# Kernel tuning notes

Measured on AMD Instinct MI355X. Metric: run time of the kernel, lower is better.

The kernel has to match this reference:

```python
import jax, jax.numpy as jnp
import numpy as np

B, L, PATCH_IN, D, NPOS = 64, 1024, 768, 1152, 256


def setup_inputs() -> dict:
    key = jax.random.key(0)
    k1, k2, k3, k4 = jax.random.split(key, 4)
    pixel_values = jax.random.normal(k1, (B, L, PATCH_IN), dtype=jnp.float32)
    # per-sample (h, w) with h*w <= L and h, w >= 16 (pure upsampling of 16x16 grid)
    hs = np.array([16 + (i % 17) for i in range(B)], dtype=np.int64)
    ws = (L // hs).astype(np.int64)
    spatial_shapes = jnp.asarray(np.stack([hs, ws], axis=1))
    W = jax.random.normal(k2, (D, PATCH_IN), dtype=jnp.float32) * 0.02
    b = jax.random.normal(k3, (D,), dtype=jnp.float32) * 0.02
    pos_emb = jax.random.normal(k4, (NPOS, D), dtype=jnp.float32) * 0.02
    return {"pixel_values": pixel_values, "spatial_shapes": spatial_shapes,
            "W": W, "b": b, "pos_emb": pos_emb}


def _resized_pos_embeddings(pos_emb, spatial_shapes_np, max_length):
    # pos_emb: [num_patches, D] -> [G, G, D] grid
    g = int(np.sqrt(pos_emb.shape[0]))
    d = pos_emb.shape[1]
    grid = pos_emb.reshape(g, g, d)
    rows = []
    for i in range(spatial_shapes_np.shape[0]):
        h, w = int(spatial_shapes_np[i, 0]), int(spatial_shapes_np[i, 1])
        # half-pixel bilinear == torch F.interpolate(align_corners=False); antialias
        # is a no-op for upsampling (h, w >= g)
        r = jax.image.resize(grid, (h, w, d), method="bilinear").reshape(h * w, d)
        pad = jnp.broadcast_to(r[0], (max_length - h * w, d))  # replicate first patch
        rows.append(jnp.concatenate([r, pad], axis=0))
    return jnp.stack(rows)  # [B, max_length, D]


def reference(pixel_values, spatial_shapes, W, b, pos_emb):
    # patch linear embedding: [B, L, Cpp] x [D, Cpp] -> [B, L, D]
    patch_embeds = jnp.einsum("blk,dk->bld", pixel_values, W) + b
    ss = np.asarray(spatial_shapes)  # static per-sample shapes
    pos = _resized_pos_embeddings(pos_emb, ss, pixel_values.shape[1])
    return patch_embeds + pos
```

## Files before the change

kernel.cpp:

```cpp
#include <hip/hip_runtime.h>

typedef __bf16 bf16x8 __attribute__((ext_vector_type(8)));
typedef float  f32x4  __attribute__((ext_vector_type(4)));

constexpr int BM = 128, BN = 128, BK = 32;
constexpr int MDIM = 65536, NDIM = 1152, KDIM = 768;
constexpr int NBN = NDIM / BN;
constexpr int NKT = KDIM / BK;
constexpr int GRID = (MDIM / BM) * NBN;
constexpr int LDSROWB = BK * 2;

__device__ __forceinline__ void gload16(const void* g, void* l) {
  __builtin_amdgcn_global_load_lds(
      (const __attribute__((address_space(1))) void*)g,
      (__attribute__((address_space(3))) void*)l, 16, 0, 0);
}

__device__ __forceinline__ unsigned pk2(float x, float y) {
  __bf16 a = (__bf16)x, b = (__bf16)y;
  return (unsigned)__builtin_bit_cast(unsigned short, a) |
         ((unsigned)__builtin_bit_cast(unsigned short, b) << 16);
}

__global__ __launch_bounds__(256)
void repack_kernel(const float* __restrict__ in, __bf16* __restrict__ out) {
  const int c    = blockIdx.x * 256 + threadIdx.x;
  const int c_in = c & 511;
  const int img  = c >> 9;
  const int kt   = img % NKT;
  const int pan  = img / NKT;
  const int o = c_in * 16;
  const int u = (o >> 6) & 7;
  const int a = o ^ ((u ^ (u >> 2)) << 4);
  const int r = a >> 6;
  const int p = (a >> 4) & 3;
  const float* src = in + (size_t)(pan * 128 + r) * KDIM + kt * 32 + p * 8;
  const float4 x = *reinterpret_cast<const float4*>(src);
  const float4 y = *reinterpret_cast<const float4*>(src + 4);
  uint4 r4;
  r4.x = pk2(x.x, x.y); r4.y = pk2(x.z, x.w);
  r4.z = pk2(y.x, y.y); r4.w = pk2(y.z, y.w);
  *reinterpret_cast<uint4*>(out + (size_t)c * 8) = r4;
}

__global__ __launch_bounds__(256, 3)
void gemm_swz2_kernel(const __bf16* __restrict__ Aimg,
                      const __bf16* __restrict__ Bimg,
                      const int*   __restrict__ ss,
                      const float* __restrict__ bias,
                      const float* __restrict__ pos,
                      float* __restrict__ out) {
  __shared__ __align__(16) unsigned char SM[32768];
  __bf16* As0 = reinterpret_cast<__bf16*>(SM);
  __bf16* Bs0 = reinterpret_cast<__bf16*>(SM + 16384);
  float*  Cs  = reinterpret_cast<float*>(SM);

  const int tid  = threadIdx.x;
  const int lane = tid & 63;
  const int wid  = tid >> 6;
  const int wr   = wid >> 1;
  const int wc   = wid & 1;

  const int bidh = blockIdx.x;
  const int bid  = (bidh & 7) * (GRID / 8) + (bidh >> 3);
  const int bm   = bid / NBN;
  const int bn   = bid % NBN;

  auto stage = [&](int kt, int buf) {
    const __bf16* wsA = Aimg + ((size_t)(bm * NKT + kt) << 12);
    const __bf16* wsB = Bimg + ((size_t)(bn * NKT + kt) << 12);
    char* la = (char*)As0 + buf * 8192;
    char* lb = (char*)Bs0 + buf * 8192;
    gload16(wsA + tid * 8,         la + tid * 16);
    gload16(wsA + (256 + tid) * 8, la + (256 + tid) * 16);
    gload16(wsB + tid * 8,         lb + tid * 16);
    gload16(wsB + (256 + tid) * 8, lb + (256 + tid) * 16);
  };

  f32x4 acc[4][4];
#pragma unroll
  for (int i = 0; i < 4; ++i)
#pragma unroll
    for (int j = 0; j < 4; ++j) acc[i][j] = (f32x4)0.0f;

  const int fr = lane & 15;
  const int kg = lane >> 4;
  const int abase = (((wr * 64 + fr) * LDSROWB) + kg * 16) ^ ((fr & 7) << 4);
  const int bbase = (((wc * 64 + fr) * LDSROWB) + kg * 16) ^ ((fr & 7) << 4);

  auto compute = [&](int buf) {
    const char* pa = (const char*)As0 + buf * 8192;
    const char* pb = (const char*)Bs0 + buf * 8192;
    bf16x8 af[4], bfv[4];
#pragma unroll
    for (int mf = 0; mf < 4; ++mf)
      af[mf] = *reinterpret_cast<const bf16x8*>(pa + abase + mf * 16 * LDSROWB);
#pragma unroll
    for (int nf = 0; nf < 4; ++nf)
      bfv[nf] = *reinterpret_cast<const bf16x8*>(pb + bbase + nf * 16 * LDSROWB);
#pragma unroll
    for (int mf = 0; mf < 4; ++mf)
#pragma unroll
      for (int nf = 0; nf < 4; ++nf)
        acc[mf][nf] = __builtin_amdgcn_mfma_f32_16x16x32_bf16(af[mf], bfv[nf], acc[mf][nf], 0, 0, 0);
  };

  stage(0, 0);
  for (int kt = 0; kt < NKT; ++kt) {
    const int cur = kt & 1;
    __syncthreads();
    if (kt + 1 < NKT) stage(kt + 1, cur ^ 1);
    compute(cur);
  }

  const int chunk = tid & 15;
  const int gcol  = bn * BN + chunk * 8;
  const f32x4 bias_lo = *reinterpret_cast<const f32x4*>(bias + gcol);
  const f32x4 bias_hi = *reinterpret_cast<const f32x4*>(bias + gcol + 4);

  const int s  = bm >> 3;
  const int h  = ss[2 * s];
  const int w  = ss[2 * s + 1];
  const int hw = h * w;
  const float rh = 16.0f / (float)h;
  const float rw = 16.0f / (float)w;

#pragma unroll
  for (int half = 0; half < 2; ++half) {
    __syncthreads();
#pragma unroll
    for (int mm = 0; mm < 2; ++mm) {
#pragma unroll
      for (int nf = 0; nf < 4; ++nf) {
#pragma unroll
        for (int rg = 0; rg < 4; ++rg) {
          const int rowL = wr * 32 + mm * 16 + kg * 4 + rg;
          const int col  = wc * 64 + nf * 16 + fr;
          const int key  = (rowL & 3) ^ ((rowL >> 2) & 3);
          Cs[(rowL << 7) + (col ^ (key << 3))] = acc[half * 2 + mm][nf][rg];
        }
      }
    }
    __syncthreads();
#pragma unroll
    for (int pass = 0; pass < 4; ++pass) {
      const int rowL = pass * 16 + (tid >> 4);
      const int key  = (rowL & 3) ^ ((rowL >> 2) & 3);
      const float* crow = Cs + (rowL << 7) + ((chunk ^ key) << 3);
      const f32x4 c0 = *reinterpret_cast<const f32x4*>(crow);
      const f32x4 c1 = *reinterpret_cast<const f32x4*>(crow + 4);

      const int grow = bm * BM + (rowL >> 5) * 64 + half * 32 + (rowL & 31);
      int p = grow & 1023;
      if (p >= hw) p = 0;
      const int y = p / w;
      const int x = p - y * w;
      const float fy = ((float)y + 0.5f) * rh - 0.5f;
      const float fx = ((float)x + 0.5f) * rw - 0.5f;
      const float yf = floorf(fy), xf = floorf(fx);
      const float ty = fy - yf,   tx = fx - xf;
      int iy0 = (int)yf, ix0 = (int)xf;
      int iy1 = iy0 + 1 > 15 ? 15 : iy0 + 1;
      int ix1 = ix0 + 1 > 15 ? 15 : ix0 + 1;
      iy0 = iy0 < 0 ? 0 : iy0;
      ix0 = ix0 < 0 ? 0 : ix0;
      const float* g00 = pos + (size_t)(iy0 * 16 + ix0) * NDIM + gcol;
      const float* g01 = pos + (size_t)(iy0 * 16 + ix1) * NDIM + gcol;
      const float* g10 = pos + (size_t)(iy1 * 16 + ix0) * NDIM + gcol;
      const float* g11 = pos + (size_t)(iy1 * 16 + ix1) * NDIM + gcol;

      const f32x4 v00l = *reinterpret_cast<const f32x4*>(g00);
      const f32x4 v01l = *reinterpret_cast<const f32x4*>(g01);
      const f32x4 v10l = *reinterpret_cast<const f32x4*>(g10);
      const f32x4 v11l = *reinterpret_cast<const f32x4*>(g11);
      const f32x4 v00h = *reinterpret_cast<const f32x4*>(g00 + 4);
      const f32x4 v01h = *reinterpret_cast<const f32x4*>(g01 + 4);
      const f32x4 v10h = *reinterpret_cast<const f32x4*>(g10 + 4);
      const f32x4 v11h = *reinterpret_cast<const f32x4*>(g11 + 4);

      const f32x4 topl = v00l + tx * (v01l - v00l);
      const f32x4 botl = v10l + tx * (v11l - v10l);
      const f32x4 pvl  = topl + ty * (botl - topl);
      const f32x4 toph = v00h + tx * (v01h - v00h);
      const f32x4 both = v10h + tx * (v11h - v10h);
      const f32x4 pvh  = toph + ty * (both - toph);

      float* orow = out + (size_t)grow * NDIM + gcol;
      *reinterpret_cast<f32x4*>(orow)     = c0 + bias_lo + pvl;
      *reinterpret_cast<f32x4*>(orow + 4) = c1 + bias_hi + pvh;
    }
  }
}

__global__ __launch_bounds__(256, 2)
void gemm_fb_kernel(const float* __restrict__ A,
                    const int*   __restrict__ ss,
                    const float* __restrict__ Wm,
                    const float* __restrict__ bias,
                    const float* __restrict__ pos,
                    float* __restrict__ out) {
  __shared__ unsigned short As[2][BM * BK];
  __shared__ unsigned short Bs[2][BM * BK];

  const int tid  = threadIdx.x;
  const int lane = tid & 63;
  const int wid  = tid >> 6;
  const int wr   = wid >> 1;
  const int wc   = wid & 1;

  const int bidh = blockIdx.x;
  const int bid  = (bidh & 7) * (GRID / 8) + (bidh >> 3);
  const int bm   = bid / NBN;
  const int bn   = bid % NBN;

  const int srow0 = tid >> 3;
  const int skc   = tid & 7;
  const float* Ag = A  + (size_t)(bm * BM + srow0) * KDIM + skc * 4;
  const float* Bg = Wm + (size_t)(bn * BN + srow0) * KDIM + skc * 4;

  float4 ra[4], rb[4];

  auto stage_load = [&](int kt) {
    const int ko = kt * BK;
#pragma unroll
    for (int r = 0; r < 4; ++r) {
      ra[r] = *reinterpret_cast<const float4*>(Ag + (size_t)(r * 32) * KDIM + ko);
      rb[r] = *reinterpret_cast<const float4*>(Bg + (size_t)(r * 32) * KDIM + ko);
    }
  };

  auto stage_write = [&](int buf) {
#pragma unroll
    for (int r = 0; r < 4; ++r) {
      const int arow = r * 32 + srow0;
      int off = arow * LDSROWB + skc * 8;
      off ^= (arow & 7) << 4;
      uint2 pa, pb;
      pa.x = pk2(ra[r].x, ra[r].y); pa.y = pk2(ra[r].z, ra[r].w);
      pb.x = pk2(rb[r].x, rb[r].y); pb.y = pk2(rb[r].z, rb[r].w);
      *reinterpret_cast<uint2*>(reinterpret_cast<char*>(&As[buf][0]) + off) = pa;
      *reinterpret_cast<uint2*>(reinterpret_cast<char*>(&Bs[buf][0]) + off) = pb;
    }
  };

  f32x4 acc[4][4];
#pragma unroll
  for (int i = 0; i < 4; ++i)
#pragma unroll
    for (int j = 0; j < 4; ++j) acc[i][j] = (f32x4)0.0f;

  const int fr = lane & 15;
  const int kg = lane >> 4;
  int abase = (wr * 64 + fr) * LDSROWB + kg * 16; abase ^= (fr & 7) << 4;
  int bbase = (wc * 64 + fr) * LDSROWB + kg * 16; bbase ^= (fr & 7) << 4;

  auto compute = [&](int buf) {
    const char* pa = reinterpret_cast<const char*>(&As[buf][0]);
    const char* pb = reinterpret_cast<const char*>(&Bs[buf][0]);
    bf16x8 af[4], bfv[4];
#pragma unroll
    for (int mf = 0; mf < 4; ++mf)
      af[mf] = *reinterpret_cast<const bf16x8*>(pa + abase + mf * 16 * LDSROWB);
#pragma unroll
    for (int nf = 0; nf < 4; ++nf)
      bfv[nf] = *reinterpret_cast<const bf16x8*>(pb + bbase + nf * 16 * LDSROWB);
#pragma unroll
    for (int mf = 0; mf < 4; ++mf)
#pragma unroll
      for (int nf = 0; nf < 4; ++nf)
        acc[mf][nf] = __builtin_amdgcn_mfma_f32_16x16x32_bf16(af[mf], bfv[nf], acc[mf][nf], 0, 0, 0);
  };

  stage_load(0);
  stage_write(0);
  for (int kt = 0; kt < NKT; ++kt) {
    const int cur = kt & 1;
    if (kt + 1 < NKT) stage_load(kt + 1);
    __syncthreads();
    compute(cur);
    if (kt + 1 < NKT) stage_write(cur ^ 1);
  }

  const int colbase = bn * BN + wc * 64 + fr;
  float bvals[4];
#pragma unroll
  for (int nf = 0; nf < 4; ++nf) bvals[nf] = bias[colbase + nf * 16];

  const int s  = bm >> 3;
  const int h  = ss[2 * s];
  const int w  = ss[2 * s + 1];
  const int hw = h * w;
  const float rh = 16.0f / (float)h;
  const float rw = 16.0f / (float)w;
  const int row0 = bm * BM + wr * 64 + kg * 4;

#pragma unroll
  for (int mf = 0; mf < 4; ++mf) {
#pragma unroll
    for (int rg = 0; rg < 4; ++rg) {
      const int row = row0 + mf * 16 + rg;
      int p = row & 1023;
      if (p >= hw) p = 0;
      const int y = p / w;
      const int x = p - y * w;
      const float fy = ((float)y + 0.5f) * rh - 0.5f;
      const float fx = ((float)x + 0.5f) * rw - 0.5f;
      const float yf = floorf(fy), xf = floorf(fx);
      const float ty = fy - yf,   tx = fx - xf;
      int iy0 = (int)yf, ix0 = (int)xf;
      int iy1 = iy0 + 1 > 15 ? 15 : iy0 + 1;
      int ix1 = ix0 + 1 > 15 ? 15 : ix0 + 1;
      iy0 = iy0 < 0 ? 0 : iy0;
      ix0 = ix0 < 0 ? 0 : ix0;
      const float* g00 = pos + (size_t)(iy0 * 16 + ix0) * NDIM;
      const float* g01 = pos + (size_t)(iy0 * 16 + ix1) * NDIM;
      const float* g10 = pos + (size_t)(iy1 * 16 + ix0) * NDIM;
      const float* g11 = pos + (size_t)(iy1 * 16 + ix1) * NDIM;
      float* orow = out + (size_t)row * NDIM;
#pragma unroll
      for (int nf = 0; nf < 4; ++nf) {
        const int col = colbase + nf * 16;
        const float p00 = g00[col], p01 = g01[col];
        const float p10 = g10[col], p11 = g11[col];
        const float top = p00 + tx * (p01 - p00);
        const float bot = p10 + tx * (p11 - p10);
        const float pv  = top + ty * (bot - top);
        orow[col] = acc[mf][nf][rg] + bvals[nf] + pv;
      }
    }
  }
}

extern "C" void kernel_launch(void* const* d_in, const int* in_sizes, int n_in,
                              void* d_out, int out_size, void* d_ws, size_t ws_size,
                              hipStream_t stream) {
  const float* A    = (const float*)d_in[0];
  const int*   ss   = (const int*)d_in[1];
  const float* Wm   = (const float*)d_in[2];
  const float* bias = (const float*)d_in[3];
  const float* pos  = (const float*)d_in[4];
  float* out = (float*)d_out;

  const size_t needA = (size_t)MDIM * KDIM * 2;
  const size_t needW = (size_t)NDIM * KDIM * 2;

  if (ws_size >= needA + needW) {
    __bf16* Ab = (__bf16*)d_ws;
    __bf16* Bb = (__bf16*)((char*)d_ws + needA);
    const int chunksA = (MDIM / 16) * NKT * 64;
    const int chunksW = (NDIM / 16) * NKT * 64;
    repack_kernel<<<chunksA / 256, 256, 0, stream>>>(A, Ab);
    repack_kernel<<<chunksW / 256, 256, 0, stream>>>(Wm, Bb);
    gemm_swz2_kernel<<<GRID, 256, 0, stream>>>(Ab, Bb, ss, bias, pos, out);
  } else {
    gemm_fb_kernel<<<GRID, 256, 0, stream>>>(A, ss, Wm, bias, pos, out);
  }
}
```

Before: 262.8 us.

## Use 8-wave 256x128 tiles with triple-buffered A pipeline and MFMA priority

Replaces the 4-wave 128x128 GEMM with an 8-wave 256x128 block that shares each B tile across two A sub-tiles. It triple-buffers A and double-buffers B, issuing loads two steps ahead with explicit vmcnt waits and barriers, and raises wave priority around the MFMA block. The epilogue writes out in four 64-row waves. The aim is to overlap global-to-LDS loads with compute and halve B traffic per output. The cost is 64KB of LDS per block, which limits occupancy, and a serialized epilogue.

```diff
diff --git a/kernel.cpp b/kernel.cpp
--- a/kernel.cpp
+++ b/kernel.cpp
@@ -3,12 +3,11 @@
 typedef __bf16 bf16x8 __attribute__((ext_vector_type(8)));
 typedef float  f32x4  __attribute__((ext_vector_type(4)));
 
-constexpr int BM = 128, BN = 128, BK = 32;
 constexpr int MDIM = 65536, NDIM = 1152, KDIM = 768;
-constexpr int NBN = NDIM / BN;
-constexpr int NKT = KDIM / BK;
-constexpr int GRID = (MDIM / BM) * NBN;
-constexpr int LDSROWB = BK * 2;
+constexpr int NBN = 9;
+constexpr int NKT = 24;
+constexpr int GRID2 = (MDIM / 256) * NBN;
+constexpr int FBGRID = (MDIM / 128) * NBN;
 
 __device__ __forceinline__ void gload16(const void* g, void* l) {
   __builtin_amdgcn_global_load_lds(
@@ -43,17 +42,15 @@
   *reinterpret_cast<uint4*>(out + (size_t)c * 8) = r4;
 }
 
-__global__ __launch_bounds__(256, 3)
-void gemm_swz2_kernel(const __bf16* __restrict__ Aimg,
-                      const __bf16* __restrict__ Bimg,
-                      const int*   __restrict__ ss,
-                      const float* __restrict__ bias,
-                      const float* __restrict__ pos,
-                      float* __restrict__ out) {
-  __shared__ __align__(16) unsigned char SM[32768];
-  __bf16* As0 = reinterpret_cast<__bf16*>(SM);
-  __bf16* Bs0 = reinterpret_cast<__bf16*>(SM + 16384);
-  float*  Cs  = reinterpret_cast<float*>(SM);
+__global__ __launch_bounds__(512, 4)
+void gemm_8w_kernel(const __bf16* __restrict__ Aimg,
+                    const __bf16* __restrict__ Bimg,
+                    const int*   __restrict__ ss,
+                    const float* __restrict__ bias,
+                    const float* __restrict__ pos,
+                    float* __restrict__ out) {
+  __shared__ __align__(16) unsigned char SM[65536];
+  char* smc = reinterpret_cast<char*>(SM);
 
   const int tid  = threadIdx.x;
   const int lane = tid & 63;
@@ -62,19 +59,20 @@
   const int wc   = wid & 1;
 
   const int bidh = blockIdx.x;
-  const int bid  = (bidh & 7) * (GRID / 8) + (bidh >> 3);
+  const int bid  = (bidh & 7) * (GRID2 / 8) + (bidh >> 3);
   const int bm   = bid / NBN;
   const int bn   = bid % NBN;
 
-  auto stage = [&](int kt, int buf) {
-    const __bf16* wsA = Aimg + ((size_t)(bm * NKT + kt) << 12);
-    const __bf16* wsB = Bimg + ((size_t)(bn * NKT + kt) << 12);
-    char* la = (char*)As0 + buf * 8192;
-    char* lb = (char*)Bs0 + buf * 8192;
-    gload16(wsA + tid * 8,         la + tid * 16);
-    gload16(wsA + (256 + tid) * 8, la + (256 + tid) * 16);
-    gload16(wsB + tid * 8,         lb + tid * 16);
-    gload16(wsB + (256 + tid) * 8, lb + (256 + tid) * 16);
+  auto stageA = [&](int kt, int abuf) {
+    const __bf16* i0 = Aimg + ((size_t)((bm * 2 + 0) * NKT + kt) << 12);
+    const __bf16* i1 = Aimg + ((size_t)((bm * 2 + 1) * NKT + kt) << 12);
+    char* d = smc + abuf * 16384;
+    gload16(i0 + tid * 8, d + tid * 16);
+    gload16(i1 + tid * 8, d + 8192 + tid * 16);
+  };
+  auto stageB = [&](int kt, int bbuf) {
+    const __bf16* ib = Bimg + ((size_t)(bn * NKT + kt) << 12);
+    gload16(ib + tid * 8, smc + 49152 + bbuf * 8192 + tid * 16);
   };
 
   f32x4 acc[4][4];
@@ -85,72 +83,96 @@
 
   const int fr = lane & 15;
   const int kg = lane >> 4;
-  const int abase = (((wr * 64 + fr) * LDSROWB) + kg * 16) ^ ((fr & 7) << 4);
-  const int bbase = (((wc * 64 + fr) * LDSROWB) + kg * 16) ^ ((fr & 7) << 4);
-
-  auto compute = [&](int buf) {
-    const char* pa = (const char*)As0 + buf * 8192;
-    const char* pb = (const char*)Bs0 + buf * 8192;
+  const int abase = (wr >> 1) * 8192 +
+                    (((((wr & 1) * 64 + fr) * 64) + kg * 16) ^ ((fr & 7) << 4));
+  const int bbase = (((wc * 64 + fr) * 64) + kg * 16) ^ ((fr & 7) << 4);
+
+  auto compute = [&](int abuf, int bbuf) {
+    const char* pa = smc + abuf * 16384 + abase;
+    const char* pb = smc + 49152 + bbuf * 8192 + bbase;
     bf16x8 af[4], bfv[4];
 #pragma unroll
     for (int mf = 0; mf < 4; ++mf)
-      af[mf] = *reinterpret_cast<const bf16x8*>(pa + abase + mf * 16 * LDSROWB);
+      af[mf] = *reinterpret_cast<const bf16x8*>(pa + mf * 1024);
 #pragma unroll
     for (int nf = 0; nf < 4; ++nf)
-      bfv[nf] = *reinterpret_cast<const bf16x8*>(pb + bbase + nf * 16 * LDSROWB);
+      bfv[nf] = *reinterpret_cast<const bf16x8*>(pb + nf * 1024);
+    __builtin_amdgcn_s_setprio(1);
 #pragma unroll
     for (int mf = 0; mf < 4; ++mf)
 #pragma unroll
       for (int nf = 0; nf < 4; ++nf)
         acc[mf][nf] = __builtin_amdgcn_mfma_f32_16x16x32_bf16(af[mf], bfv[nf], acc[mf][nf], 0, 0, 0);
-  };
-
-  stage(0, 0);
-  for (int kt = 0; kt < NKT; ++kt) {
-    const int cur = kt & 1;
-    __syncthreads();
-    if (kt + 1 < NKT) stage(kt + 1, cur ^ 1);
-    compute(cur);
-  }
-
+    __builtin_amdgcn_s_setprio(0);
+  };
+
+#define K_ITER(KT, AB, BB, IA, IB, VMS)                                  \
+  {                                                                      \
+    asm volatile("s_waitcnt vmcnt(" VMS ")" ::: "memory");               \
+    __builtin_amdgcn_s_barrier();                                        \
+    __builtin_amdgcn_sched_barrier(0);                                   \
+    if (IB) stageB((KT) + 1, ((KT) + 1) & 1);                            \
+    if (IA) stageA((KT) + 2, ((KT) + 2) % 3);                            \
+    compute(AB, BB);                                                     \
+  }
+
+  stageA(0, 0);
+  stageB(0, 0);
+  stageA(1, 1);
+  for (int k6 = 0; k6 < 18; k6 += 6) {
+    K_ITER(k6 + 0, 0, 0, true, true, "2");
+    K_ITER(k6 + 1, 1, 1, true, true, "2");
+    K_ITER(k6 + 2, 2, 0, true, true, "2");
+    K_ITER(k6 + 3, 0, 1, true, true, "2");
+    K_ITER(k6 + 4, 1, 0, true, true, "2");
+    K_ITER(k6 + 5, 2, 1, true, true, "2");
+  }
+  K_ITER(18, 0, 0, true,  true,  "2");
+  K_ITER(19, 1, 1, true,  true,  "2");
+  K_ITER(20, 2, 0, true,  true,  "2");
+  K_ITER(21, 0, 1, true,  true,  "2");
+  K_ITER(22, 1, 0, false, true,  "2");
+  K_ITER(23, 2, 1, false, false, "0");
+#undef K_ITER
+
+  float* Cs = reinterpret_cast<float*>(SM);
   const int chunk = tid & 15;
-  const int gcol  = bn * BN + chunk * 8;
+  const int gcol  = bn * 128 + chunk * 8;
   const f32x4 bias_lo = *reinterpret_cast<const f32x4*>(bias + gcol);
   const f32x4 bias_hi = *reinterpret_cast<const f32x4*>(bias + gcol + 4);
 
-  const int s  = bm >> 3;
-  const int h  = ss[2 * s];
-  const int w  = ss[2 * s + 1];
+  const int sidx = bm >> 2;
+  const int h  = ss[2 * sidx];
+  const int w  = ss[2 * sidx + 1];
   const int hw = h * w;
   const float rh = 16.0f / (float)h;
   const float rw = 16.0f / (float)w;
 
-#pragma unroll
-  for (int half = 0; half < 2; ++half) {
+  for (int sw = 0; sw < 4; ++sw) {
     __syncthreads();
-#pragma unroll
-    for (int mm = 0; mm < 2; ++mm) {
-#pragma unroll
-      for (int nf = 0; nf < 4; ++nf) {
-#pragma unroll
-        for (int rg = 0; rg < 4; ++rg) {
-          const int rowL = wr * 32 + mm * 16 + kg * 4 + rg;
-          const int col  = wc * 64 + nf * 16 + fr;
-          const int key  = (rowL & 3) ^ ((rowL >> 2) & 3);
-          Cs[(rowL << 7) + (col ^ (key << 3))] = acc[half * 2 + mm][nf][rg];
-        }
-      }
+    if (wr == sw) {
+#pragma unroll
+      for (int mf = 0; mf < 4; ++mf)
+#pragma unroll
+        for (int nf = 0; nf < 4; ++nf)
+#pragma unroll
+          for (int rg = 0; rg < 4; ++rg) {
+            const int rowL = mf * 16 + kg * 4 + rg;
+            const int col  = wc * 64 + nf * 16 + fr;
+            const int key  = (rowL & 3) ^ ((rowL >> 2) & 3);
+            Cs[(rowL << 7) + (col ^ (key << 3))] = acc[mf][nf][rg];
+          }
     }
     __syncthreads();
 #pragma unroll
-    for (int pass = 0; pass < 4; ++pass) {
-      const int rowL = pass * 16 + (tid >> 4);
+    for (int pass = 0; pass < 2; ++pass) {
+      const int rowL = pass * 32 + (tid >> 4);
       const int key  = (rowL & 3) ^ ((rowL >> 2) & 3);
       const float* crow = Cs + (rowL << 7) + ((chunk ^ key) << 3);
       const f32x4 c0 = *reinterpret_cast<const f32x4*>(crow);
       const f32x4 c1 = *reinterpret_cast<const f32x4*>(crow + 4);
 
-      const int grow = bm * BM + (rowL >> 5) * 64 + half * 32 + (rowL & 31);
+      const int grow = bm * 256 + sw * 64 + rowL;
       int p = grow & 1023;
       if (p >= hw) p = 0;
       const int y = p / w;
@@ -199,8 +221,8 @@
                     const float* __restrict__ bias,
                     const float* __restrict__ pos,
                     float* __restrict__ out) {
-  __shared__ unsigned short As[2][BM * BK];
-  __shared__ unsigned short Bs[2][BM * BK];
+  __shared__ unsigned short As[2][128 * 32];
+  __shared__ unsigned short Bs[2][128 * 32];
 
   const int tid  = threadIdx.x;
   const int lane = tid & 63;
@@ -209,19 +231,19 @@
   const int wc   = wid & 1;
 
   const int bidh = blockIdx.x;
-  const int bid  = (bidh & 7) * (GRID / 8) + (bidh >> 3);
+  const int bid  = (bidh & 7) * (FBGRID / 8) + (bidh >> 3);
   const int bm   = bid / NBN;
   const int bn   = bid % NBN;
 
   const int srow0 = tid >> 3;
   const int skc   = tid & 7;
-  const float* Ag = A  + (size_t)(bm * BM + srow0) * KDIM + skc * 4;
-  const float* Bg = Wm + (size_t)(bn * BN + srow0) * KDIM + skc * 4;
+  const float* Ag = A  + (size_t)(bm * 128 + srow0) * KDIM + skc * 4;
+  const float* Bg = Wm + (size_t)(bn * 128 + srow0) * KDIM + skc * 4;
 
   float4 ra[4], rb[4];
 
   auto stage_load = [&](int kt) {
-    const int ko = kt * BK;
+    const int ko = kt * 32;
 #pragma unroll
     for (int r = 0; r < 4; ++r) {
       ra[r] = *reinterpret_cast<const float4*>(Ag + (size_t)(r * 32) * KDIM + ko);
@@ -233,7 +255,7 @@
 #pragma unroll
     for (int r = 0; r < 4; ++r) {
       const int arow = r * 32 + srow0;
-      int off = arow * LDSROWB + skc * 8;
+      int off = arow * 64 + skc * 8;
       off ^= (arow & 7) << 4;
       uint2 pa, pb;
       pa.x = pk2(ra[r].x, ra[r].y); pa.y = pk2(ra[r].z, ra[r].w);
@@ -251,8 +273,8 @@
 
   const int fr = lane & 15;
   const int kg = lane >> 4;
-  int abase = (wr * 64 + fr) * LDSROWB + kg * 16; abase ^= (fr & 7) << 4;
-  int bbase = (wc * 64 + fr) * LDSROWB + kg * 16; bbase ^= (fr & 7) << 4;
+  int abase = (wr * 64 + fr) * 64 + kg * 16; abase ^= (fr & 7) << 4;
+  int bbase = (wc * 64 + fr) * 64 + kg * 16; bbase ^= (fr & 7) << 4;
 
   auto compute = [&](int buf) {
     const char* pa = reinterpret_cast<const char*>(&As[buf][0]);
@@ -260,10 +282,10 @@
     bf16x8 af[4], bfv[4];
 #pragma unroll
     for (int mf = 0; mf < 4; ++mf)
-      af[mf] = *reinterpret_cast<const bf16x8*>(pa + abase + mf * 16 * LDSROWB);
+      af[mf] = *reinterpret_cast<const bf16x8*>(pa + abase + mf * 16 * 64);
 #pragma unroll
     for (int nf = 0; nf < 4; ++nf)
-      bfv[nf] = *reinterpret_cast<const bf16x8*>(pb + bbase + nf * 16 * LDSROWB);
+      bfv[nf] = *reinterpret_cast<const bf16x8*>(pb + bbase + nf * 16 * 64);
 #pragma unroll
     for (int mf = 0; mf < 4; ++mf)
 #pragma unroll
@@ -281,7 +303,7 @@
     if (kt + 1 < NKT) stage_write(cur ^ 1);
   }
 
-  const int colbase = bn * BN + wc * 64 + fr;
+  const int colbase = bn * 128 + wc * 64 + fr;
   float bvals[4];
 #pragma unroll
   for (int nf = 0; nf < 4; ++nf) bvals[nf] = bias[colbase + nf * 16];
@@ -292,7 +314,7 @@
   const int hw = h * w;
   const float rh = 16.0f / (float)h;
   const float rw = 16.0f / (float)w;
-  const int row0 = bm * BM + wr * 64 + kg * 4;
+  const int row0 = bm * 128 + wr * 64 + kg * 4;
 
 #pragma unroll
   for (int mf = 0; mf < 4; ++mf) {
@@ -351,8 +373,8 @@
     const int chunksW = (NDIM / 16) * NKT * 64;
     repack_kernel<<<chunksA / 256, 256, 0, stream>>>(A, Ab);
     repack_kernel<<<chunksW / 256, 256, 0, stream>>>(Wm, Bb);
-    gemm_swz2_kernel<<<GRID, 256, 0, stream>>>(Ab, Bb, ss, bias, pos, out);
+    gemm_8w_kernel<<<GRID2, 512, 0, stream>>>(Ab, Bb, ss, bias, pos, out);
   } else {
-    gemm_fb_kernel<<<GRID, 256, 0, stream>>>(A, ss, Wm, bias, pos, out);
-  }
-}
+    gemm_fb_kernel<<<FBGRID, 256, 0, stream>>>(A, ss, Wm, bias, pos, out);
+  }
+}
```

New measurement: 281.5 us. 1.07x slower.
